# Performance work log

Measured on AMD Instinct MI355X. Metric: run time of the kernel, lower is better.

Reference implementation:

```python
import jax, jax.numpy as jnp
import numpy as np

MEM_DIM = 1024
N_CHILD = 16384

def _linear_params(key, out_dim, in_dim):
    kw, kb = jax.random.split(key)
    bound = 1.0 / np.sqrt(in_dim)
    W = jax.random.uniform(kw, (out_dim, in_dim), jnp.float32, -bound, bound)
    b = jax.random.uniform(kb, (out_dim,), jnp.float32, -bound, bound)
    return W, b

def setup_inputs() -> dict:
    key = jax.random.key(0)
    ks = jax.random.split(key, 7)
    child_c = jax.random.normal(ks[0], (N_CHILD, MEM_DIM), jnp.float32)
    child_h = jax.random.normal(ks[1], (N_CHILD, MEM_DIM), jnp.float32)
    child_h_sum = jax.random.normal(ks[2], (MEM_DIM,), jnp.float32)
    W_ih, b_ih = _linear_params(ks[3], MEM_DIM, MEM_DIM)
    W_fh, b_fh = _linear_params(ks[4], MEM_DIM, MEM_DIM)
    W_uh, b_uh = _linear_params(ks[5], MEM_DIM, MEM_DIM)
    W_oh, b_oh = _linear_params(ks[6], MEM_DIM, MEM_DIM)
    return {
        "child_c": child_c, "child_h": child_h, "child_h_sum": child_h_sum,
        "W_ih": W_ih, "b_ih": b_ih, "W_fh": W_fh, "b_fh": b_fh,
        "W_uh": W_uh, "b_uh": b_uh, "W_oh": W_oh, "b_oh": b_oh,
    }

def reference(child_c, child_h, child_h_sum,
              W_ih, b_ih, W_fh, b_fh, W_uh, b_uh, W_oh, b_oh):
    # Gate projections on the summed child hidden state: [mem_dim]
    i = jax.nn.sigmoid(child_h_sum @ W_ih.T + b_ih)
    o = jax.nn.sigmoid(child_h_sum @ W_oh.T + b_oh)
    u = jnp.tanh(child_h_sum @ W_uh.T + b_uh)
    # Per-child forget gates, batched (replaces the Python loop): [N, mem_dim]
    f = jax.nn.sigmoid(child_h @ W_fh.T + b_fh)
    fc = f * child_c                     # [N, mem_dim]
    c = i * u + jnp.sum(fc, axis=0)      # [mem_dim]
    h = o * jnp.tanh(c)                  # [mem_dim]
    return (c, h)
```

## Files before the change

### kernel.cpp

```cpp
#include <hip/hip_runtime.h>
#include <hip/hip_bf16.h>
#include <math.h>

#define MEM_DIM 1024
#define N_CHILD 16384

#define BM 128
#define BN 128
#define BK 64
#define KITERS (MEM_DIM / BK)

typedef __bf16 bf16_t;
typedef __bf16 bf16x4 __attribute__((ext_vector_type(4)));
typedef __bf16 bf16x8 __attribute__((ext_vector_type(8)));
typedef float f32x4 __attribute__((ext_vector_type(4)));

__device__ __forceinline__ void async_load16(const bf16_t* g, bf16_t* l) {
    __builtin_amdgcn_global_load_lds(
        (const __attribute__((address_space(1))) unsigned int*)g,
        (__attribute__((address_space(3))) unsigned int*)l,
        16, 0, 0);
}

__global__ __launch_bounds__(256) void cvt_bf16_kernel(const float* __restrict__ src,
                                                       bf16_t* __restrict__ dst, int n8) {
    int t = blockIdx.x * 256 + threadIdx.x;
    if (t < n8) {
        const float4* s = (const float4*)src + (size_t)t * 2;
        float4 a = s[0], b = s[1];
        bf16x8 o = { (bf16_t)a.x, (bf16_t)a.y, (bf16_t)a.z, (bf16_t)a.w,
                     (bf16_t)b.x, (bf16_t)b.y, (bf16_t)b.z, (bf16_t)b.w };
        *(bf16x8*)(dst + (size_t)t * 8) = o;
    }
}

__global__ void gates_kernel(const float* __restrict__ hsum,
                             const float* __restrict__ W_ih, const float* __restrict__ b_ih,
                             const float* __restrict__ W_uh, const float* __restrict__ b_uh,
                             const float* __restrict__ W_oh, const float* __restrict__ b_oh,
                             float* __restrict__ acc_c, float* __restrict__ o_ws) {
    const int j = blockIdx.x;
    const int tid = threadIdx.x;
    const float* wi = W_ih + (size_t)j * MEM_DIM;
    const float* wu = W_uh + (size_t)j * MEM_DIM;
    const float* wo = W_oh + (size_t)j * MEM_DIM;
    float si = 0.f, su = 0.f, so = 0.f;
    for (int k = tid; k < MEM_DIM; k += 256) {
        float hv = hsum[k];
        si += wi[k] * hv;
        su += wu[k] * hv;
        so += wo[k] * hv;
    }
    for (int off = 32; off > 0; off >>= 1) {
        si += __shfl_down(si, off, 64);
        su += __shfl_down(su, off, 64);
        so += __shfl_down(so, off, 64);
    }
    __shared__ float red[3][4];
    const int wave = tid >> 6, lane = tid & 63;
    if (lane == 0) { red[0][wave] = si; red[1][wave] = su; red[2][wave] = so; }
    __syncthreads();
    if (tid == 0) {
        float ti = red[0][0] + red[0][1] + red[0][2] + red[0][3] + b_ih[j];
        float tu = red[1][0] + red[1][1] + red[1][2] + red[1][3] + b_uh[j];
        float to = red[2][0] + red[2][1] + red[2][2] + red[2][3] + b_oh[j];
        float iv = 1.f / (1.f + expf(-ti));
        float uv = tanhf(tu);
        float ov = 1.f / (1.f + expf(-to));
        acc_c[j] = iv * uv;
        o_ws[j]  = ov;
    }
}

__global__ __launch_bounds__(256) void fused_gemm_bf16(
        const bf16_t* __restrict__ hbf, const bf16_t* __restrict__ wbf,
        const float* __restrict__ child_c, const float* __restrict__ b_fh,
        float* __restrict__ acc_c) {
    __shared__ __align__(1024) bf16_t sA[BM * BK];
    __shared__ __align__(1024) bf16_t sB[BN * BK];
    __shared__ float sred[BN];

    const int tid  = threadIdx.x;
    const int lane = tid & 63;
    const int wave = tid >> 6;
    const int wr = wave >> 1, wc = wave & 1;
    const int q  = lane >> 4;
    const int cl = lane & 15;

    const int b   = blockIdx.x;
    const int xcd = b & 7;
    const int l   = b >> 3;
    const int jt  = l & 7;
    const int ntl = l >> 3;
    const int j0  = jt * BN;
    const int n0  = (xcd * 16 + ntl) * BM;

    const int rl = lane >> 3;
    const int p  = lane & 7;
    const int cf = (p ^ rl) * 8;
    const bf16_t* gA[4];
    const bf16_t* gB[4];
    bf16_t* lA[4];
    bf16_t* lB[4];
#pragma unroll
    for (int i = 0; i < 4; i++) {
        const int r = wave * 32 + i * 8 + rl;
        gA[i] = hbf + (size_t)(n0 + r) * MEM_DIM + cf;
        gB[i] = wbf + (size_t)(j0 + r) * MEM_DIM + cf;
        lA[i] = &sA[(wave * 32 + i * 8) * BK];
        lB[i] = &sB[(wave * 32 + i * 8) * BK];
    }

    f32x4 acc[4][4];
#pragma unroll
    for (int a = 0; a < 4; a++)
#pragma unroll
        for (int c = 0; c < 4; c++) acc[a][c] = (f32x4)0.0f;

    for (int k = 0; k < KITERS; ++k) {
#pragma unroll
        for (int i = 0; i < 4; i++) {
            async_load16(gA[i], lA[i]);
            async_load16(gB[i], lB[i]);
            gA[i] += BK; gB[i] += BK;
        }
        __syncthreads();

#pragma unroll
        for (int h = 0; h < 2; h++) {
            bf16x8 af[4], bfr[4];
#pragma unroll
            for (int mt = 0; mt < 4; mt++) {
                const int ra = wr * 64 + mt * 16 + cl;
                const int rb = wc * 64 + mt * 16 + cl;
                af[mt]  = *(const bf16x8*)(&sA[ra * BK + (((4 * h + q) ^ (cl & 7)) * 8)]);
                bfr[mt] = *(const bf16x8*)(&sB[rb * BK + (((4 * h + q) ^ (cl & 7)) * 8)]);
            }
#pragma unroll
            for (int mt = 0; mt < 4; mt++)
#pragma unroll
                for (int nt = 0; nt < 4; nt++)
                    acc[mt][nt] = __builtin_amdgcn_mfma_f32_16x16x32_bf16(
                        af[mt], bfr[nt], acc[mt][nt], 0, 0, 0);
        }
        __syncthreads();
    }

    if (tid < BN) sred[tid] = 0.0f;
    __syncthreads();

    float colsum[4] = {0.f, 0.f, 0.f, 0.f};
#pragma unroll
    for (int nt = 0; nt < 4; nt++) {
        const int col = j0 + wc * 64 + nt * 16 + cl;
        const float bias = b_fh[col];
#pragma unroll
        for (int mt = 0; mt < 4; mt++) {
#pragma unroll
            for (int r = 0; r < 4; r++) {
                const int row = n0 + wr * 64 + mt * 16 + q * 4 + r;
                float s = acc[mt][nt][r] + bias;
                float fg = 1.0f / (1.0f + __expf(-s));
                colsum[nt] += fg * child_c[(size_t)row * MEM_DIM + col];
            }
        }
        colsum[nt] += __shfl_xor(colsum[nt], 16, 64);
        colsum[nt] += __shfl_xor(colsum[nt], 32, 64);
    }
    if (q == 0) {
#pragma unroll
        for (int nt = 0; nt < 4; nt++)
            atomicAdd(&sred[wc * 64 + nt * 16 + cl], colsum[nt]);
    }
    __syncthreads();
    if (tid < BN) atomicAdd(&acc_c[j0 + tid], sred[tid]);
}

#define LDS_STRIDE 40
__global__ __launch_bounds__(256) void fused_gemm_f32(
        const float* __restrict__ child_h, const float* __restrict__ child_c,
        const float* __restrict__ W_fh, const float* __restrict__ b_fh,
        float* __restrict__ acc_c) {
    __shared__ __align__(16) bf16_t sA[BM * LDS_STRIDE];
    __shared__ __align__(16) bf16_t sB[BN * LDS_STRIDE];
    __shared__ float sred[BN];
    const int tid = threadIdx.x, lane = tid & 63, wave = tid >> 6;
    const int wr = wave >> 1, wc = wave & 1;
    const int j0 = blockIdx.x * BN, n0 = blockIdx.y * BM;
    const int q = lane >> 4, cl = lane & 15;
    f32x4 acc[4][4];
#pragma unroll
    for (int a = 0; a < 4; a++)
#pragma unroll
        for (int c = 0; c < 4; c++) acc[a][c] = (f32x4)0.0f;
    for (int k0 = 0; k0 < MEM_DIM; k0 += 32) {
#pragma unroll
        for (int i = 0; i < 4; i++) {
            int f = tid + i * 256, row = f >> 3, col = (f & 7) * 4;
            float4 va = *(const float4*)(child_h + (size_t)(n0 + row) * MEM_DIM + k0 + col);
            float4 vb = *(const float4*)(W_fh    + (size_t)(j0 + row) * MEM_DIM + k0 + col);
            bf16x4 ba = { (bf16_t)va.x, (bf16_t)va.y, (bf16_t)va.z, (bf16_t)va.w };
            bf16x4 bb = { (bf16_t)vb.x, (bf16_t)vb.y, (bf16_t)vb.z, (bf16_t)vb.w };
            *(bf16x4*)(&sA[row * LDS_STRIDE + col]) = ba;
            *(bf16x4*)(&sB[row * LDS_STRIDE + col]) = bb;
        }
        __syncthreads();
        bf16x8 af[4], bfr[4];
#pragma unroll
        for (int mt = 0; mt < 4; mt++) {
            af[mt]  = *(const bf16x8*)(&sA[(wr * 64 + mt * 16 + cl) * LDS_STRIDE + q * 8]);
            bfr[mt] = *(const bf16x8*)(&sB[(wc * 64 + mt * 16 + cl) * LDS_STRIDE + q * 8]);
        }
#pragma unroll
        for (int mt = 0; mt < 4; mt++)
#pragma unroll
            for (int nt = 0; nt < 4; nt++)
                acc[mt][nt] = __builtin_amdgcn_mfma_f32_16x16x32_bf16(af[mt], bfr[nt], acc[mt][nt], 0, 0, 0);
        __syncthreads();
    }
    if (tid < BN) sred[tid] = 0.0f;
    __syncthreads();
    float colsum[4] = {0.f, 0.f, 0.f, 0.f};
#pragma unroll
    for (int nt = 0; nt < 4; nt++) {
        const int col = j0 + wc * 64 + nt * 16 + cl;
        const float bias = b_fh[col];
#pragma unroll
        for (int mt = 0; mt < 4; mt++)
#pragma unroll
            for (int r = 0; r < 4; r++) {
                const int row = n0 + wr * 64 + mt * 16 + q * 4 + r;
                float s = acc[mt][nt][r] + bias;
                float fg = 1.0f / (1.0f + __expf(-s));
                colsum[nt] += fg * child_c[(size_t)row * MEM_DIM + col];
            }
        colsum[nt] += __shfl_xor(colsum[nt], 16, 64);
        colsum[nt] += __shfl_xor(colsum[nt], 32, 64);
    }
    if (q == 0)
#pragma unroll
        for (int nt = 0; nt < 4; nt++)
            atomicAdd(&sred[wc * 64 + nt * 16 + cl], colsum[nt]);
    __syncthreads();
    if (tid < BN) atomicAdd(&acc_c[j0 + tid], sred[tid]);
}

__global__ void finalize_kernel(const float* __restrict__ acc_c,
                                const float* __restrict__ o_ws,
                                float* __restrict__ out) {
    int t = blockIdx.x * 256 + threadIdx.x;
    if (t < MEM_DIM) {
        float cv = acc_c[t];
        float hv = o_ws[t] * tanhf(cv);
        out[t] = cv;
        out[MEM_DIM + t] = hv;
    }
}

extern "C" void kernel_launch(void* const* d_in, const int* in_sizes, int n_in,
                              void* d_out, int out_size, void* d_ws, size_t ws_size,
                              hipStream_t stream) {
    const float* child_c = (const float*)d_in[0];
    const float* child_h = (const float*)d_in[1];
    const float* hsum    = (const float*)d_in[2];
    const float* W_ih    = (const float*)d_in[3];
    const float* b_ih    = (const float*)d_in[4];
    const float* W_fh    = (const float*)d_in[5];
    const float* b_fh    = (const float*)d_in[6];
    const float* W_uh    = (const float*)d_in[7];
    const float* b_uh    = (const float*)d_in[8];
    const float* W_oh    = (const float*)d_in[9];
    const float* b_oh    = (const float*)d_in[10];
    float* out   = (float*)d_out;

    float* acc_c = (float*)d_ws;
    float* o_ws  = acc_c + MEM_DIM;
    const size_t HBF_OFF = 8192;
    const size_t HBF_BYTES = (size_t)N_CHILD * MEM_DIM * 2;
    const size_t WBF_BYTES = (size_t)MEM_DIM * MEM_DIM * 2;
    const size_t NEED = HBF_OFF + HBF_BYTES + WBF_BYTES;

    gates_kernel<<<MEM_DIM, 256, 0, stream>>>(hsum, W_ih, b_ih, W_uh, b_uh, W_oh, b_oh,
                                              acc_c, o_ws);

    if (ws_size >= NEED) {
        bf16_t* hbf = (bf16_t*)((char*)d_ws + HBF_OFF);
        bf16_t* wbf = (bf16_t*)((char*)d_ws + HBF_OFF + HBF_BYTES);
        int n8_h = (N_CHILD * MEM_DIM) / 8;
        int n8_w = (MEM_DIM * MEM_DIM) / 8;
        cvt_bf16_kernel<<<(n8_h + 255) / 256, 256, 0, stream>>>(child_h, hbf, n8_h);
        cvt_bf16_kernel<<<(n8_w + 255) / 256, 256, 0, stream>>>(W_fh, wbf, n8_w);
        fused_gemm_bf16<<<(N_CHILD / BM) * (MEM_DIM / BN), 256, 0, stream>>>(
            hbf, wbf, child_c, b_fh, acc_c);
    } else {
        dim3 grid(MEM_DIM / BN, N_CHILD / BM);
        fused_gemm_f32<<<grid, 256, 0, stream>>>(child_h, child_c, W_fh, b_fh, acc_c);
    }
    finalize_kernel<<<(MEM_DIM + 255) / 256, 256, 0, stream>>>(acc_c, o_ws, out);
}
```

Measured before the change: 218.9 us.

## Merge gates and bf16 conversion into one prep kernel, finalize via last-block counter

Combines the gate GEMV kernel and both bf16 conversion launches into a single prep kernel that branches on block index. The finalize step moves into the GEMM kernel: each block bumps a global counter, and the last block to finish computes c and h. The GEMM also gains a launch-bounds occupancy hint of 3. The aim is to cut launch count from five to two and remove the inter-kernel gaps, at the cost of an extra threadfence and atomic per block plus a serial tail in the last block.

```diff
diff --git a/kernel.cpp b/kernel.cpp
--- a/kernel.cpp
+++ b/kernel.cpp
@@ -9,6 +9,7 @@
 #define BN 128
 #define BK 64
 #define KITERS (MEM_DIM / BK)
+#define GEMM_BLOCKS ((N_CHILD / BM) * (MEM_DIM / BN))
 
 typedef __bf16 bf16_t;
 typedef __bf16 bf16x4 __attribute__((ext_vector_type(4)));
@@ -22,15 +23,179 @@
         16, 0, 0);
 }
 
-__global__ __launch_bounds__(256) void cvt_bf16_kernel(const float* __restrict__ src,
-                                                       bf16_t* __restrict__ dst, int n8) {
-    int t = blockIdx.x * 256 + threadIdx.x;
-    if (t < n8) {
-        const float4* s = (const float4*)src + (size_t)t * 2;
-        float4 a = s[0], b = s[1];
-        bf16x8 o = { (bf16_t)a.x, (bf16_t)a.y, (bf16_t)a.z, (bf16_t)a.w,
-                     (bf16_t)b.x, (bf16_t)b.y, (bf16_t)b.z, (bf16_t)b.w };
-        *(bf16x8*)(dst + (size_t)t * 8) = o;
+__global__ __launch_bounds__(256) void prep_kernel(
+        const float* __restrict__ child_h, const float* __restrict__ W_fh,
+        bf16_t* __restrict__ dst, int n8,
+        const float* __restrict__ hsum,
+        const float* __restrict__ W_ih, const float* __restrict__ b_ih,
+        const float* __restrict__ W_uh, const float* __restrict__ b_uh,
+        const float* __restrict__ W_oh, const float* __restrict__ b_oh,
+        float* __restrict__ acc_c, float* __restrict__ o_ws, int* __restrict__ ctr) {
+    const int tid = threadIdx.x;
+    if (blockIdx.x < MEM_DIM) {
+        const int j = blockIdx.x;
+        if (j == 0 && tid == 0) *ctr = 0;
+        const float* wi = W_ih + (size_t)j * MEM_DIM;
+        const float* wu = W_uh + (size_t)j * MEM_DIM;
+        const float* wo = W_oh + (size_t)j * MEM_DIM;
+        float si = 0.f, su = 0.f, so = 0.f;
+        for (int k = tid; k < MEM_DIM; k += 256) {
+            float hv = hsum[k];
+            si += wi[k] * hv;
+            su += wu[k] * hv;
+            so += wo[k] * hv;
+        }
+        for (int off = 32; off > 0; off >>= 1) {
+            si += __shfl_down(si, off, 64);
+            su += __shfl_down(su, off, 64);
+            so += __shfl_down(so, off, 64);
+        }
+        __shared__ float red[3][4];
+        const int wave = tid >> 6, lane = tid & 63;
+        if (lane == 0) { red[0][wave] = si; red[1][wave] = su; red[2][wave] = so; }
+        __syncthreads();
+        if (tid == 0) {
+            float ti = red[0][0] + red[0][1] + red[0][2] + red[0][3] + b_ih[j];
+            float tu = red[1][0] + red[1][1] + red[1][2] + red[1][3] + b_uh[j];
+            float to = red[2][0] + red[2][1] + red[2][2] + red[2][3] + b_oh[j];
+            float iv = 1.f / (1.f + expf(-ti));
+            float uv = tanhf(tu);
+            float ov = 1.f / (1.f + expf(-to));
+            acc_c[j] = iv * uv;
+            o_ws[j]  = ov;
+        }
+    } else {
+        const int nA8 = (N_CHILD * MEM_DIM) / 8;
+        int t = (blockIdx.x - MEM_DIM) * 256 + tid;
+        if (t < n8) {
+            const float* s = (t < nA8) ? (child_h + (size_t)t * 8)
+                                       : (W_fh + (size_t)(t - nA8) * 8);
+            float4 a = *(const float4*)s;
+            float4 b = *(const float4*)(s + 4);
+            bf16x8 o = { (bf16_t)a.x, (bf16_t)a.y, (bf16_t)a.z, (bf16_t)a.w,
+                         (bf16_t)b.x, (bf16_t)b.y, (bf16_t)b.z, (bf16_t)b.w };
+            *(bf16x8*)(dst + (size_t)t * 8) = o;
+        }
+    }
+}
+
+__global__ __launch_bounds__(256, 3) void fused_gemm_bf16(
+        const bf16_t* __restrict__ hbf, const bf16_t* __restrict__ wbf,
+        const float* __restrict__ child_c, const float* __restrict__ b_fh,
+        float* __restrict__ acc_c, const float* __restrict__ o_ws,
+        int* __restrict__ ctr, float* __restrict__ out) {
+    __shared__ __align__(1024) bf16_t sA[BM * BK];
+    __shared__ __align__(1024) bf16_t sB[BN * BK];
+    __shared__ float sred[BN];
+    __shared__ int slast;
+
+    const int tid  = threadIdx.x;
+    const int lane = tid & 63;
+    const int wave = tid >> 6;
+    const int wr = wave >> 1, wc = wave & 1;
+    const int q  = lane >> 4;
+    const int cl = lane & 15;
+
+    const int b   = blockIdx.x;
+    const int xcd = b & 7;
+    const int l   = b >> 3;
+    const int jt  = l & 7;
+    const int ntl = l >> 3;
+    const int j0  = jt * BN;
+    const int n0  = (xcd * 16 + ntl) * BM;
+
+    const int rl = lane >> 3;
+    const int p  = lane & 7;
+    const int cf = (p ^ rl) * 8;
+    const bf16_t* gA[4];
+    const bf16_t* gB[4];
+    bf16_t* lA[4];
+    bf16_t* lB[4];
+#pragma unroll
+    for (int i = 0; i < 4; i++) {
+        const int r = wave * 32 + i * 8 + rl;
+        gA[i] = hbf + (size_t)(n0 + r) * MEM_DIM + cf;
+        gB[i] = wbf + (size_t)(j0 + r) * MEM_DIM + cf;
+        lA[i] = &sA[(wave * 32 + i * 8) * BK];
+        lB[i] = &sB[(wave * 32 + i * 8) * BK];
+    }
+
+    f32x4 acc[4][4];
+#pragma unroll
+    for (int a = 0; a < 4; a++)
+#pragma unroll
+        for (int c = 0; c < 4; c++) acc[a][c] = (f32x4)0.0f;
+
+    for (int k = 0; k < KITERS; ++k) {
+#pragma unroll
+        for (int i = 0; i < 4; i++) {
+            async_load16(gA[i], lA[i]);
+            async_load16(gB[i], lB[i]);
+            gA[i] += BK; gB[i] += BK;
+        }
+        __syncthreads();
+
+#pragma unroll
+        for (int h = 0; h < 2; h++) {
+            bf16x8 af[4], bfr[4];
+#pragma unroll
+            for (int mt = 0; mt < 4; mt++) {
+                const int ra = wr * 64 + mt * 16 + cl;
+                const int rb = wc * 64 + mt * 16 + cl;
+                af[mt]  = *(const bf16x8*)(&sA[ra * BK + (((4 * h + q) ^ (cl & 7)) * 8)]);
+                bfr[mt] = *(const bf16x8*)(&sB[rb * BK + (((4 * h + q) ^ (cl & 7)) * 8)]);
+            }
+#pragma unroll
+            for (int mt = 0; mt < 4; mt++)
+#pragma unroll
+                for (int nt = 0; nt < 4; nt++)
+                    acc[mt][nt] = __builtin_amdgcn_mfma_f32_16x16x32_bf16(
+                        af[mt], bfr[nt], acc[mt][nt], 0, 0, 0);
+        }
+        __syncthreads();
+    }
+
+    if (tid < BN) sred[tid] = 0.0f;
+    __syncthreads();
+
+    float colsum[4] = {0.f, 0.f, 0.f, 0.f};
+#pragma unroll
+    for (int nt = 0; nt < 4; nt++) {
+        const int col = j0 + wc * 64 + nt * 16 + cl;
+        const float bias = b_fh[col];
+#pragma unroll
+        for (int mt = 0; mt < 4; mt++) {
+#pragma unroll
+            for (int r = 0; r < 4; r++) {
+                const int row = n0 + wr * 64 + mt * 16 + q * 4 + r;
+                float s = acc[mt][nt][r] + bias;
+                float fg = 1.0f / (1.0f + __expf(-s));
+                colsum[nt] += fg * child_c[(size_t)row * MEM_DIM + col];
+            }
+        }
+        colsum[nt] += __shfl_xor(colsum[nt], 16, 64);
+        colsum[nt] += __shfl_xor(colsum[nt], 32, 64);
+    }
+    if (q == 0) {
+#pragma unroll
+        for (int nt = 0; nt < 4; nt++)
+            atomicAdd(&sred[wc * 64 + nt * 16 + cl], colsum[nt]);
+    }
+    __syncthreads();
+    if (tid < BN) atomicAdd(&acc_c[j0 + tid], sred[tid]);
+
+    __threadfence();
+    __syncthreads();
+    if (tid == 0) slast = atomicAdd(ctr, 1);
+    __syncthreads();
+    if (slast == GEMM_BLOCKS - 1) {
+        __threadfence();
+        for (int j = tid; j < MEM_DIM; j += 256) {
+            float cv = atomicAdd(&acc_c[j], 0.0f);
+            float hv = o_ws[j] * tanhf(cv);
+            out[j] = cv;
+            out[MEM_DIM + j] = hv;
+        }
     }
 }
 
@@ -64,116 +229,9 @@
         float ti = red[0][0] + red[0][1] + red[0][2] + red[0][3] + b_ih[j];
         float tu = red[1][0] + red[1][1] + red[1][2] + red[1][3] + b_uh[j];
         float to = red[2][0] + red[2][1] + red[2][2] + red[2][3] + b_oh[j];
-        float iv = 1.f / (1.f + expf(-ti));
-        float uv = tanhf(tu);
-        float ov = 1.f / (1.f + expf(-to));
-        acc_c[j] = iv * uv;
-        o_ws[j]  = ov;
-    }
-}
-
-__global__ __launch_bounds__(256) void fused_gemm_bf16(
-        const bf16_t* __restrict__ hbf, const bf16_t* __restrict__ wbf,
-        const float* __restrict__ child_c, const float* __restrict__ b_fh,
-        float* __restrict__ acc_c) {
-    __shared__ __align__(1024) bf16_t sA[BM * BK];
-    __shared__ __align__(1024) bf16_t sB[BN * BK];
-    __shared__ float sred[BN];
-
-    const int tid  = threadIdx.x;
-    const int lane = tid & 63;
-    const int wave = tid >> 6;
-    const int wr = wave >> 1, wc = wave & 1;
-    const int q  = lane >> 4;
-    const int cl = lane & 15;
-
-    const int b   = blockIdx.x;
-    const int xcd = b & 7;
-    const int l   = b >> 3;
-    const int jt  = l & 7;
-    const int ntl = l >> 3;
-    const int j0  = jt * BN;
-    const int n0  = (xcd * 16 + ntl) * BM;
-
-    const int rl = lane >> 3;
-    const int p  = lane & 7;
-    const int cf = (p ^ rl) * 8;
-    const bf16_t* gA[4];
-    const bf16_t* gB[4];
-    bf16_t* lA[4];
-    bf16_t* lB[4];
-#pragma unroll
-    for (int i = 0; i < 4; i++) {
-        const int r = wave * 32 + i * 8 + rl;
-        gA[i] = hbf + (size_t)(n0 + r) * MEM_DIM + cf;
-        gB[i] = wbf + (size_t)(j0 + r) * MEM_DIM + cf;
-        lA[i] = &sA[(wave * 32 + i * 8) * BK];
-        lB[i] = &sB[(wave * 32 + i * 8) * BK];
-    }
-
-    f32x4 acc[4][4];
-#pragma unroll
-    for (int a = 0; a < 4; a++)
-#pragma unroll
-        for (int c = 0; c < 4; c++) acc[a][c] = (f32x4)0.0f;
-
-    for (int k = 0; k < KITERS; ++k) {
-#pragma unroll
-        for (int i = 0; i < 4; i++) {
-            async_load16(gA[i], lA[i]);
-            async_load16(gB[i], lB[i]);
-            gA[i] += BK; gB[i] += BK;
-        }
-        __syncthreads();
-
-#pragma unroll
-        for (int h = 0; h < 2; h++) {
-            bf16x8 af[4], bfr[4];
-#pragma unroll
-            for (int mt = 0; mt < 4; mt++) {
-                const int ra = wr * 64 + mt * 16 + cl;
-                const int rb = wc * 64 + mt * 16 + cl;
-                af[mt]  = *(const bf16x8*)(&sA[ra * BK + (((4 * h + q) ^ (cl & 7)) * 8)]);
-                bfr[mt] = *(const bf16x8*)(&sB[rb * BK + (((4 * h + q) ^ (cl & 7)) * 8)]);
-            }
-#pragma unroll
-            for (int mt = 0; mt < 4; mt++)
-#pragma unroll
-                for (int nt = 0; nt < 4; nt++)
-                    acc[mt][nt] = __builtin_amdgcn_mfma_f32_16x16x32_bf16(
-                        af[mt], bfr[nt], acc[mt][nt], 0, 0, 0);
-        }
-        __syncthreads();
-    }
-
-    if (tid < BN) sred[tid] = 0.0f;
-    __syncthreads();
-
-    float colsum[4] = {0.f, 0.f, 0.f, 0.f};
-#pragma unroll
-    for (int nt = 0; nt < 4; nt++) {
-        const int col = j0 + wc * 64 + nt * 16 + cl;
-        const float bias = b_fh[col];
-#pragma unroll
-        for (int mt = 0; mt < 4; mt++) {
-#pragma unroll
-            for (int r = 0; r < 4; r++) {
-                const int row = n0 + wr * 64 + mt * 16 + q * 4 + r;
-                float s = acc[mt][nt][r] + bias;
-                float fg = 1.0f / (1.0f + __expf(-s));
-                colsum[nt] += fg * child_c[(size_t)row * MEM_DIM + col];
-            }
-        }
-        colsum[nt] += __shfl_xor(colsum[nt], 16, 64);
-        colsum[nt] += __shfl_xor(colsum[nt], 32, 64);
-    }
-    if (q == 0) {
-#pragma unroll
-        for (int nt = 0; nt < 4; nt++)
-            atomicAdd(&sred[wc * 64 + nt * 16 + cl], colsum[nt]);
-    }
-    __syncthreads();
-    if (tid < BN) atomicAdd(&acc_c[j0 + tid], sred[tid]);
+        acc_c[j] = (1.f / (1.f + expf(-ti))) * tanhf(tu);
+        o_ws[j]  = 1.f / (1.f + expf(-to));
+    }
 }
 
 #define LDS_STRIDE 40
@@ -181,12 +239,12 @@
         const float* __restrict__ child_h, const float* __restrict__ child_c,
         const float* __restrict__ W_fh, const float* __restrict__ b_fh,
         float* __restrict__ acc_c) {
-    __shared__ __align__(16) bf16_t sA[BM * LDS_STRIDE];
-    __shared__ __align__(16) bf16_t sB[BN * LDS_STRIDE];
-    __shared__ float sred[BN];
+    __shared__ __align__(16) bf16_t sA[128 * LDS_STRIDE];
+    __shared__ __align__(16) bf16_t sB[128 * LDS_STRIDE];
+    __shared__ float sred[128];
     const int tid = threadIdx.x, lane = tid & 63, wave = tid >> 6;
     const int wr = wave >> 1, wc = wave & 1;
-    const int j0 = blockIdx.x * BN, n0 = blockIdx.y * BM;
+    const int j0 = blockIdx.x * 128, n0 = blockIdx.y * 128;
     const int q = lane >> 4, cl = lane & 15;
     f32x4 acc[4][4];
 #pragma unroll
@@ -218,7 +276,7 @@
                 acc[mt][nt] = __builtin_amdgcn_mfma_f32_16x16x32_bf16(af[mt], bfr[nt], acc[mt][nt], 0, 0, 0);
         __syncthreads();
     }
-    if (tid < BN) sred[tid] = 0.0f;
+    if (tid < 128) sred[tid] = 0.0f;
     __syncthreads();
     float colsum[4] = {0.f, 0.f, 0.f, 0.f};
 #pragma unroll
@@ -242,7 +300,7 @@
         for (int nt = 0; nt < 4; nt++)
             atomicAdd(&sred[wc * 64 + nt * 16 + cl], colsum[nt]);
     __syncthreads();
-    if (tid < BN) atomicAdd(&acc_c[j0 + tid], sred[tid]);
+    if (tid < 128) atomicAdd(&acc_c[j0 + tid], sred[tid]);
 }
 
 __global__ void finalize_kernel(const float* __restrict__ acc_c,
@@ -275,26 +333,27 @@
 
     float* acc_c = (float*)d_ws;
     float* o_ws  = acc_c + MEM_DIM;
-    const size_t HBF_OFF = 8192;
+    int*   ctr   = (int*)((char*)d_ws + 8192);
+    const size_t HBF_OFF   = 12288;
     const size_t HBF_BYTES = (size_t)N_CHILD * MEM_DIM * 2;
     const size_t WBF_BYTES = (size_t)MEM_DIM * MEM_DIM * 2;
     const size_t NEED = HBF_OFF + HBF_BYTES + WBF_BYTES;
 
-    gates_kernel<<<MEM_DIM, 256, 0, stream>>>(hsum, W_ih, b_ih, W_uh, b_uh, W_oh, b_oh,
-                                              acc_c, o_ws);
-
     if (ws_size >= NEED) {
         bf16_t* hbf = (bf16_t*)((char*)d_ws + HBF_OFF);
-        bf16_t* wbf = (bf16_t*)((char*)d_ws + HBF_OFF + HBF_BYTES);
-        int n8_h = (N_CHILD * MEM_DIM) / 8;
-        int n8_w = (MEM_DIM * MEM_DIM) / 8;
-        cvt_bf16_kernel<<<(n8_h + 255) / 256, 256, 0, stream>>>(child_h, hbf, n8_h);
-        cvt_bf16_kernel<<<(n8_w + 255) / 256, 256, 0, stream>>>(W_fh, wbf, n8_w);
-        fused_gemm_bf16<<<(N_CHILD / BM) * (MEM_DIM / BN), 256, 0, stream>>>(
-            hbf, wbf, child_c, b_fh, acc_c);
+        bf16_t* wbf = hbf + (size_t)N_CHILD * MEM_DIM;
+        const int n8 = (N_CHILD * MEM_DIM + MEM_DIM * MEM_DIM) / 8;
+        const int cvtBlocks = (n8 + 255) / 256;
+        prep_kernel<<<MEM_DIM + cvtBlocks, 256, 0, stream>>>(
+            child_h, W_fh, hbf, n8,
+            hsum, W_ih, b_ih, W_uh, b_uh, W_oh, b_oh, acc_c, o_ws, ctr);
+        fused_gemm_bf16<<<GEMM_BLOCKS, 256, 0, stream>>>(
+            hbf, wbf, child_c, b_fh, acc_c, o_ws, ctr, out);
     } else {
-        dim3 grid(MEM_DIM / BN, N_CHILD / BM);
+        gates_kernel<<<MEM_DIM, 256, 0, stream>>>(hsum, W_ih, b_ih, W_uh, b_uh,
+                                                  W_oh, b_oh, acc_c, o_ws);
+        dim3 grid(MEM_DIM / 128, N_CHILD / 128);
         fused_gemm_f32<<<grid, 256, 0, stream>>>(child_h, child_c, W_fh, b_fh, acc_c);
-    }
-    finalize_kernel<<<(MEM_DIM + 255) / 256, 256, 0, stream>>>(acc_c, o_ws, out);
-}
+        finalize_kernel<<<(MEM_DIM + 255) / 256, 256, 0, stream>>>(acc_c, o_ws, out);
+    }
+}
```

Result: slower. 320.3 us (+46.3%).
